# Kernel optimization log

Measured on AMD Instinct MI355X. Metric: run time of the kernel, lower is better.

Reference implementation:

```python
import jax, jax.numpy as jnp
import numpy as np

N, H, K, B, L = 8192, 256, 128, 64, 128


def setup_inputs() -> dict:
    key = jax.random.key(0)
    ks = jax.random.split(key, 12)
    s_emb = 1.0 / np.sqrt(H)
    return {
        "A": jax.random.normal(ks[0], (N, N), jnp.float32) * 0.02,           # dense adjacency
        "emb": jax.random.normal(ks[1], (N, H), jnp.float32) * s_emb,        # GCN embedding
        "Wc": jax.random.normal(ks[2], (H, H), jnp.float32) * s_emb,         # Conv1d k=1 (multi_gram)
        "bc": jnp.zeros((H,), jnp.float32),
        "W1": jax.random.normal(ks[3], (K, 2 * H), jnp.float32) * 0.05,      # Conv2d fs=1, width=2H
        "b1": jnp.zeros((K,), jnp.float32),
        "W2": jax.random.normal(ks[4], (K, 2, 2 * H), jnp.float32) * 0.05,   # Conv2d fs=2
        "b2": jnp.zeros((K,), jnp.float32),
        "Wd": jax.random.normal(ks[5], (2, 4 * K), jnp.float32) * 0.05,      # dense
        "bd": jnp.zeros((2,), jnp.float32),
        "q_idx": jax.random.randint(ks[6], (B, L), 0, N, jnp.int32),
        "a_idx": jax.random.randint(ks[7], (B, L), 0, N, jnp.int32),
    }


def reference(A, emb, Wc, bc, W1, b1, W2, b2, Wd, bd, q_idx, a_idx):
    # GCN layer (featureless): layer1 = A @ embedding  -> [N, H]
    layer1 = A @ emb

    # padded per-sample word gather + multi_gram (kernel-1 conv == rowwise linear + ReLU)
    def gram(idx):
        x = jnp.take(layer1, idx, axis=0)                      # [B, L, H]
        return jax.nn.relu(jnp.einsum("blh,oh->blo", x, Wc) + bc)

    Qm = gram(q_idx)                                           # [B, L, H]
    Am = gram(a_idx)                                           # [B, L, H]

    # soft cross attention
    s = jnp.einsum("bqh,bkh->bqk", Qm, Am)                     # [B, Lq, La]
    eq = jnp.einsum("bqk,bkh->bqh", jax.nn.softmax(s, axis=-1), Am)
    ea = jnp.einsum("bkq,bqh->bkh", jax.nn.softmax(jnp.swapaxes(s, 1, 2), axis=-1), Qm)

    # full-width conv2d encoders over [L, 2H] feature map, max-pooled over L
    def encode(X, E):
        t = jnp.concatenate([(X - E) ** 2, X * E], axis=-1)    # [B, L, 2H]
        e1 = jax.nn.relu(jnp.einsum("bld,kd->blk", t, W1) + b1).max(axis=1)      # fs=1 -> [B, K]
        e2 = jax.nn.relu(
            jnp.einsum("bld,kd->blk", t[:, :-1], W2[:, 0])
            + jnp.einsum("bld,kd->blk", t[:, 1:], W2[:, 1])
            + b2
        ).max(axis=1)                                          # fs=2 -> [B, K]
        return jax.nn.relu(jnp.concatenate([e1, e2], axis=-1)) # [B, 2K] (dropout = identity in eval)

    re = jnp.concatenate([encode(Qm, eq), encode(Am, ea)], axis=-1)  # [B, 4K]
    return jax.nn.log_softmax(re @ Wd.T + bd, axis=-1)          # [B, 2]
```

## Files before the change

kernel.cpp:

```cpp
#include <hip/hip_runtime.h>
#include <hip/hip_bf16.h>
#include <math.h>

#define NN 8192
#define HH 256
#define BB 64
#define LL 128
#define SPLITK 4

typedef __attribute__((ext_vector_type(8))) short short8v;
typedef __attribute__((ext_vector_type(4))) short short4v;
typedef __attribute__((ext_vector_type(4))) float f32x4;

static __device__ inline short bf16bits(float f) {
    __hip_bfloat16 h = __float2bfloat16(f);
    return __builtin_bit_cast(short, h);
}
static __device__ inline float bits2f(short s) {
    __hip_bfloat16 h = __builtin_bit_cast(__hip_bfloat16, s);
    return __bfloat162float(h);
}
static __device__ inline short8v cvt8(float4 f0, float4 f1) {
    short8v r;
    r[0] = bf16bits(f0.x); r[1] = bf16bits(f0.y);
    r[2] = bf16bits(f0.z); r[3] = bf16bits(f0.w);
    r[4] = bf16bits(f1.x); r[5] = bf16bits(f1.y);
    r[6] = bf16bits(f1.z); r[7] = bf16bits(f1.w);
    return r;
}
static __device__ inline void glds16(const void* src, void* lds) {
    __builtin_amdgcn_global_load_lds(
        (const __attribute__((address_space(1))) void*)src,
        (__attribute__((address_space(3))) void*)lds, 16, 0, 0);
}
template<int N> static __device__ inline void vmwait() {
    if constexpr (N == 0)  asm volatile("s_waitcnt vmcnt(0)"  ::: "memory");
    else if constexpr (N == 1)  asm volatile("s_waitcnt vmcnt(1)"  ::: "memory");
    else if constexpr (N == 2)  asm volatile("s_waitcnt vmcnt(2)"  ::: "memory");
    else if constexpr (N == 3)  asm volatile("s_waitcnt vmcnt(3)"  ::: "memory");
    else if constexpr (N == 4)  asm volatile("s_waitcnt vmcnt(4)"  ::: "memory");
    else if constexpr (N == 5)  asm volatile("s_waitcnt vmcnt(5)"  ::: "memory");
    else if constexpr (N == 6)  asm volatile("s_waitcnt vmcnt(6)"  ::: "memory");
    else if constexpr (N == 7)  asm volatile("s_waitcnt vmcnt(7)"  ::: "memory");
    else if constexpr (N == 8)  asm volatile("s_waitcnt vmcnt(8)"  ::: "memory");
    else                        asm volatile("s_waitcnt vmcnt(12)" ::: "memory");
}
static __device__ inline void lgkm0_barrier() {
    asm volatile("s_waitcnt lgkmcnt(0)" ::: "memory");
    __builtin_amdgcn_s_barrier();
    __builtin_amdgcn_sched_barrier(0);
}


__global__ __launch_bounds__(256) void prep(
    const float* __restrict__ emb, short* __restrict__ embT,
    const float* __restrict__ Wc, short* __restrict__ Wcb,
    const float* __restrict__ W1, const float* __restrict__ W2,
    short* __restrict__ WcatT)
{
    __shared__ short tile[64][65];
    const int bid = blockIdx.x;
    const int t = threadIdx.x;
    if (bid < 512) {
        const int k0 = (bid & 127) * 64, h0 = (bid >> 7) * 64;
#pragma unroll
        for (int i = 0; i < 16; i++) {
            int idx = t + i * 256;
            int k = idx >> 6, h = idx & 63;
            tile[h][k] = bf16bits(emb[(long)(k0 + k) * 256 + h0 + h]);
        }
        __syncthreads();
#pragma unroll
        for (int i = 0; i < 16; i++) {
            int idx = t + i * 256;
            int h = idx >> 6, k = idx & 63;
            int n = h0 + h;
            int kk = (k0 + k) ^ ((n & 3) << 3);
            embT[(long)n * NN + kk] = tile[h][k];
        }
    } else {
        int i = (bid - 512) * 256 + t;
        if (i < 256 * 256) {
            int n = i >> 8, c = i & 255;
            Wcb[n * 256 + (c ^ ((n & 3) << 3))] = bf16bits(Wc[i]);
        }
        if (i < 384 * 512) {
            int n = i >> 9, d = i & 511;
            float v;
            if (n < 128)      v = W1[n * 512 + d];
            else if (n < 256) v = W2[(n - 128) * 1024 + d];
            else              v = W2[(n - 256) * 1024 + 512 + d];
            WcatT[n * 512 + (d ^ ((n & 3) << 3))] = bf16bits(v);
        }
    }
}

__global__ __launch_bounds__(512, 4) void l1_gemm(
    const float* __restrict__ Af, const short* __restrict__ Bt,
    short* __restrict__ Part)
{
    constexpr int AST = 40;

    __shared__ short As[2][128 * AST];
    __shared__ short Bs[3][256 * 32];

    const int tid = threadIdx.x;
    const int wave = tid >> 6, lane = tid & 63;
    const int wr = wave >> 2, wc = wave & 3;
    const int r16 = lane & 15, kg = lane >> 4;

    const int sk = blockIdx.x & 3, mt = blockIdx.x >> 2;
    const int m0 = mt * 128;
    const int kbeg = sk * 2048;
    constexpr int NIT = 64;

    const int arow = tid >> 2;
    const int akc = (tid & 3) * 8;
    const long arow_g = (long)(m0 + arow) * NN;

    f32x4 acc[4][4] = {};

#define STAGE_B(T, BUF)                                                        \
    {                                                                          \
        const int kt_ = kbeg + (T) * 32;                                       \
        _Pragma("unroll")                                                      \
        for (int c = 0; c < 2; c++) {                                          \
            int chunk = c * 512 + tid;                                         \
            int n_ = chunk >> 2, kc_ = (chunk & 3) * 8;                        \
            glds16(Bt + (long)n_ * NN + kt_ + kc_,                             \
                   &Bs[BUF][(c * 512 + wave * 64) * 8]);                       \
        }                                                                      \
    }
#define LOAD_A(T, F0, F1)                                                      \
    {                                                                          \
        const float* ap_ = Af + arow_g + kbeg + (T) * 32 + akc;                \
        (F0) = *(const float4*)ap_; (F1) = *(const float4*)(ap_ + 4);          \
    }
#define WRITE_A(BUF, F0, F1) { *(short8v*)&As[BUF][arow * AST + akc] = cvt8((F0), (F1)); }

    float4 p0f0, p0f1, c1f0, c1f1;
    LOAD_A(0, p0f0, p0f1);  STAGE_B(0, 0);
    LOAD_A(1, c1f0, c1f1);  STAGE_B(1, 1);
    WRITE_A(0, p0f0, p0f1);
    vmwait<4>();
    lgkm0_barrier();

    for (int t = 0; t < NIT; ++t) {
        const int curA = t & 1, nwA = (t + 1) & 1;
        const int curB = t % 3, nsB = (t + 2) % 3;
        float4 nf0, nf1;
        if (t + 2 < NIT) {
            LOAD_A(t + 2, nf0, nf1);
            STAGE_B(t + 2, nsB);
        }

        short8v a[4], b[4];
#pragma unroll
        for (int i = 0; i < 4; i++)
            a[i] = *(const short8v*)&As[curA][(wr * 64 + i * 16 + r16) * AST + kg * 8];
#pragma unroll
        for (int j = 0; j < 4; j++) {
            int n = wc * 64 + j * 16 + r16;
            b[j] = *(const short8v*)&Bs[curB][n * 32 + ((kg * 8) ^ ((n & 3) << 3))];
        }
#pragma unroll
        for (int i = 0; i < 4; i++)
#pragma unroll
            for (int j = 0; j < 4; j++)
                acc[i][j] = __builtin_amdgcn_mfma_f32_16x16x32_bf16(
                    a[i], b[j], acc[i][j], 0, 0, 0);

        if (t + 1 < NIT) {
            WRITE_A(nwA, c1f0, c1f1);
            if (t + 2 < NIT) vmwait<4>();
            else             vmwait<0>();
            lgkm0_barrier();
        }
        c1f0 = nf0; c1f1 = nf1;
    }
#undef STAGE_B
#undef LOAD_A
#undef WRITE_A

    short* P = Part + (long)sk * NN * HH;
#pragma unroll
    for (int i = 0; i < 4; i++)
#pragma unroll
        for (int j = 0; j < 4; j++) {
            int col = wc * 64 + j * 16 + r16;
#pragma unroll
            for (int r = 0; r < 4; r++) {
                int row = m0 + wr * 64 + i * 16 + kg * 4 + r;
                P[(long)row * HH + col] = bf16bits(acc[i][j][r]);
            }
        }
}

__global__ __launch_bounds__(256) void reduceK(
    const short* __restrict__ P, short* __restrict__ out)
{
    const long n = (long)NN * HH;
    long i = ((long)blockIdx.x * 256 + threadIdx.x) * 8;
    if (i >= n) return;
    float acc[8] = {};
#pragma unroll
    for (int k = 0; k < SPLITK; k++) {
        short8v v = *(const short8v*)&P[(long)k * n + i];
#pragma unroll
        for (int j = 0; j < 8; j++) acc[j] += bits2f(v[j]);
    }
    short8v o;
#pragma unroll
    for (int j = 0; j < 8; j++) o[j] = bf16bits(acc[j]);
    *(short8v*)&out[i] = o;
}

template<int NW, int NT, int GATHER, int EPI>
__global__ __launch_bounds__(256) void gemm_small(
    const short* __restrict__ Aq, const short* __restrict__ Aa,
    const short* __restrict__ Bt,
    float* __restrict__ Cfq, float* __restrict__ Cfa,
    short* __restrict__ Cbq, short* __restrict__ Cba,
    short* __restrict__ Ctq, short* __restrict__ Cta,
    const float* __restrict__ bias,
    const int* __restrict__ idxq, const int* __restrict__ idxa,
    int M, int N, int Kd)
{
    constexpr int BM = 64;
    constexpr int BN = NW * 4;
    constexpr int NB = NW / 16;
    constexpr int BCALLS = BN / BM;
    constexpr int OPS = 1 + BCALLS;
    constexpr int AST = 40;

    __shared__ short As[4][BM * AST];
    __shared__ short Bs[4][BN * 32];

    const int tid = threadIdx.x;
    const int wave = tid >> 6, lane = tid & 63;
    const int wc = wave & 3;
    const int r16 = lane & 15, kg = lane >> 4;

    const int bid = blockIdx.x;
    const int side = bid & 1;
    const int nt = (bid >> 1) & (NT - 1);
    const int mt = bid >> (NT == 2 ? 2 : 1);
    const int m0 = mt * BM;
    const int n0 = nt * BN;
    const int niter = Kd / 32;

    const short* Ab = side ? Aa : Aq;
    const int* rowidx = side ? idxa : idxq;

    const int arow = tid >> 2;
    const int akc = (tid & 3) * 8;
    long arow_g;
    { int r = GATHER ? rowidx[m0 + arow] : (m0 + arow); arow_g = (long)r * Kd; }

    f32x4 acc[4][NB] = {};

#define STAGE_B(T, BUF)                                                        \
    {                                                                          \
        const int kt_ = (T) * 32;                                              \
        _Pragma("unroll")                                                      \
        for (int c = 0; c < BCALLS; c++) {                                     \
            int chunk = c * 256 + tid;                                         \
            int n_ = chunk >> 2, kc_ = (chunk & 3) * 8;                        \
            glds16(Bt + (long)(n0 + n_) * Kd + kt_ + kc_,                      \
                   &Bs[BUF][(c * 256 + wave * 64) * 8]);                       \
        }                                                                      \
    }
#define LOAD_A(T, AR)  { (AR) = *(const short8v*)(Ab + arow_g + (T) * 32 + akc); }
#define WRITE_A(BUF, AR) { *(short8v*)&As[BUF][arow * AST + akc] = (AR); }

    short8v a0, a1, a2;
    LOAD_A(0, a0);  STAGE_B(0, 0);
    LOAD_A(1, a1);  STAGE_B(1, 1);
    LOAD_A(2, a2);  STAGE_B(2, 2);
    WRITE_A(0, a0);
    vmwait<2 * OPS>();
    lgkm0_barrier();

    for (int t = 0; t < niter; ++t) {
        const int cur = t & 3, nw = (t + 1) & 3, ns = (t + 3) & 3;
        short8v na;
        if (t + 3 < niter) {
            LOAD_A(t + 3, na);
            STAGE_B(t + 3, ns);
        }

        short8v a[4], b[NB];
#pragma unroll
        for (int i = 0; i < 4; i++)
            a[i] = *(const short8v*)&As[cur][(i * 16 + r16) * AST + kg * 8];
#pragma unroll
        for (int j = 0; j < NB; j++) {
            int n = wc * NW + j * 16 + r16;
            b[j] = *(const short8v*)&Bs[cur][n * 32 + ((kg * 8) ^ ((n & 3) << 3))];
        }
#pragma unroll
        for (int i = 0; i < 4; i++)
#pragma unroll
            for (int j = 0; j < NB; j++)
                acc[i][j] = __builtin_amdgcn_mfma_f32_16x16x32_bf16(
                    a[i], b[j], acc[i][j], 0, 0, 0);

        if (t + 1 < niter) {
            WRITE_A(nw, a1);
            if (t + 3 < niter)      vmwait<2 * OPS>();
            else if (t + 2 < niter) vmwait<OPS>();
            else                    vmwait<0>();
            lgkm0_barrier();
        }
        a1 = a2; a2 = na;
    }
#undef STAGE_B
#undef LOAD_A
#undef WRITE_A

    if (EPI == 2) {
        float* Cf = side ? Cfa : Cfq;
#pragma unroll
        for (int i = 0; i < 4; i++)
#pragma unroll
            for (int j = 0; j < NB; j++) {
                int col = n0 + wc * NW + j * 16 + r16;
#pragma unroll
                for (int r = 0; r < 4; r++) {
                    int row = m0 + i * 16 + kg * 4 + r;
                    Cf[(long)row * N + col] = acc[i][j][r];
                }
            }
    } else {
        short* Cb = side ? Cba : Cbq;
        short* Ct = side ? Cta : Ctq;
#pragma unroll
        for (int i = 0; i < 4; i++)
#pragma unroll
            for (int j = 0; j < NB; j++) {
                int col = n0 + wc * NW + j * 16 + r16;
                float bv = bias[col];
                float vr[4];
#pragma unroll
                for (int r = 0; r < 4; r++)
                    vr[r] = fmaxf(acc[i][j][r] + bv, 0.f);
                int rbase = m0 + i * 16 + kg * 4;
                int bb = rbase >> 7;
                int lbase = rbase & 127;
#pragma unroll
                for (int r = 0; r < 4; r++) {
                    int grow = rbase + r;
                    Cb[(long)grow * 256 + (col ^ ((grow & 7) << 3))] = bf16bits(vr[r]);
                }
                short4v t4;
#pragma unroll
                for (int r = 0; r < 4; r++) t4[r] = bf16bits(vr[r]);
                int lsw = lbase ^ ((col & 7) << 3);
                *(short4v*)&Ct[(long)bb * (256 * 128) + col * 128 + lsw] = t4;
            }
    }
}

__global__ __launch_bounds__(256) void qkT(
    const short* __restrict__ Qb16, const short* __restrict__ Ab16,
    float* __restrict__ s)
{
    __shared__ short Q[64 * 256];
    __shared__ short Am[128 * 256];
    const int b = blockIdx.x >> 1;
    const int qh = blockIdx.x & 1;
    const int tid = threadIdx.x, wave = tid >> 6, lane = tid & 63;
    const int r16 = lane & 15, kg = lane >> 4;
    const long boff = (long)b * 128 * 256;
    const long qoff = boff + (long)qh * 64 * 256;

#pragma unroll
    for (int c = 0; c < 8; c++)
        glds16(Qb16 + qoff + ((long)c * 256 + tid) * 8, &Q[(c * 256 + wave * 64) * 8]);
#pragma unroll
    for (int c = 0; c < 16; c++)
        glds16(Ab16 + boff + ((long)c * 256 + tid) * 8, &Am[(c * 256 + wave * 64) * 8]);
    __syncthreads();

    f32x4 acc[8] = {};
    const int q0 = wave * 16;
#pragma unroll
    for (int ks = 0; ks < 8; ks++) {
        short8v a;
        {
            int q = q0 + r16;
            a = *(const short8v*)&Q[q * 256 + ((ks * 32 + kg * 8) ^ ((q & 7) << 3))];
        }
#pragma unroll
        for (int j = 0; j < 8; j++) {
            int n = j * 16 + r16;
            short8v bf = *(const short8v*)&Am[n * 256 + ((ks * 32 + kg * 8) ^ ((n & 7) << 3))];
            acc[j] = __builtin_amdgcn_mfma_f32_16x16x32_bf16(a, bf, acc[j], 0, 0, 0);
        }
    }

    float* sp = s + (long)b * 16384 + (long)qh * 64 * 128;
#pragma unroll
    for (int j = 0; j < 8; j++)
#pragma unroll
        for (int r = 0; r < 4; r++) {
            int q = q0 + kg * 4 + r;
            int k = j * 16 + r16;
            sp[q * 128 + k] = acc[j][r];
        }
}

__global__ __launch_bounds__(256) void attn_pv(
    const float* __restrict__ s,
    const short* __restrict__ AT, const short* __restrict__ QT,
    const short* __restrict__ Qb16, const short* __restrict__ Ab16,
    short* __restrict__ t_q, short* __restrict__ t_a)
{
    __shared__ short XL[256 * 128];
    __shared__ float sm[64 * 128];
    __shared__ short P[64 * 128];
    const int b = blockIdx.x >> 2;
    const int side = (blockIdx.x >> 1) & 1;
    const int h = blockIdx.x & 1;
    const int tid = threadIdx.x, wave = tid >> 6, lane = tid & 63;
    const int r16 = lane & 15, kg = lane >> 4;

    const short* XT   = side ? QT : AT;
    const short* Xrow = side ? Ab16 : Qb16;
    short* tout       = side ? t_a : t_q;

#pragma unroll
    for (int c = 0; c < 16; c++)
        glds16(XT + (long)b * 32768 + ((long)c * 256 + tid) * 8,
               &XL[(c * 256 + wave * 64) * 8]);
    if (side == 0) {
#pragma unroll
        for (int c = 0; c < 8; c++)
            glds16(s + (long)b * 16384 + (long)h * 8192 + ((long)c * 256 + tid) * 4,
                   &sm[(c * 256 + wave * 64) * 4]);
    } else {
#pragma unroll
        for (int c = 0; c < 8; c++) {
            int idx = c * 256 + tid;
            int q = idx >> 4, off = (idx & 15) * 4;
            glds16(s + (long)b * 16384 + (long)q * 128 + h * 64 + off,
                   &sm[(c * 256 + wave * 64) * 4]);
        }
    }
    __syncthreads();

    {
        const int r = tid >> 2;
        const int qt = tid & 3;
        float mx = -1e30f;
#pragma unroll 8
        for (int i = 0; i < 32; i++) {
            int k = qt * 32 + ((i + r) & 31);
            float v = (side == 0) ? sm[r * 128 + k] : sm[k * 64 + r];
            mx = fmaxf(mx, v);
        }
        mx = fmaxf(mx, __shfl_xor(mx, 1));
        mx = fmaxf(mx, __shfl_xor(mx, 2));
        float sum = 0.f;
#pragma unroll 8
        for (int i = 0; i < 32; i++) {
            int k = qt * 32 + ((i + r) & 31);
            float v = (side == 0) ? sm[r * 128 + k] : sm[k * 64 + r];
            sum += __expf(v - mx);
        }
        sum += __shfl_xor(sum, 1);
        sum += __shfl_xor(sum, 2);
        float inv = 1.f / sum;
#pragma unroll 8
        for (int i = 0; i < 32; i++) {
            int k = qt * 32 + ((i + r) & 31);
            float v = (side == 0) ? sm[r * 128 + k] : sm[k * 64 + r];
            P[r * 128 + (k ^ ((r & 7) << 3))] = bf16bits(__expf(v - mx) * inv);
        }
    }
    __syncthreads();

    f32x4 acc[4][4] = {};
#pragma unroll
    for (int ks = 0; ks < 4; ks++) {
        short8v a[4], bf[4];
#pragma unroll
        for (int i = 0; i < 4; i++) {
            int row = i * 16 + r16;
            a[i] = *(const short8v*)&P[row * 128 + ((ks * 32 + kg * 8) ^ ((row & 7) << 3))];
        }
#pragma unroll
        for (int j = 0; j < 4; j++) {
            int hh = wave * 64 + j * 16 + r16;
            bf[j] = *(const short8v*)&XL[hh * 128 + ((ks * 32 + kg * 8) ^ ((hh & 7) << 3))];
        }
#pragma unroll
        for (int i = 0; i < 4; i++)
#pragma unroll
            for (int j = 0; j < 4; j++)
                acc[i][j] = __builtin_amdgcn_mfma_f32_16x16x32_bf16(
                    a[i], bf[j], acc[i][j], 0, 0, 0);
    }

    short* tp = tout + (long)b * 128 * 512 + (long)h * 64 * 512;
    const short* xr = Xrow + (long)b * 128 * 256 + (long)h * 64 * 256;
#pragma unroll
    for (int i = 0; i < 4; i++)
#pragma unroll
        for (int j = 0; j < 4; j++) {
            int col = wave * 64 + j * 16 + r16;
#pragma unroll
            for (int r = 0; r < 4; r++) {
                int row = i * 16 + kg * 4 + r;
                float E = acc[i][j][r];
                float x = bits2f(xr[row * 256 + (col ^ ((row & 7) << 3))]);
                float d = x - E;
                tp[(long)row * 512 + col] = bf16bits(d * d);
                tp[(long)row * 512 + 256 + col] = bf16bits(x * E);
            }
        }
}

__global__ __launch_bounds__(512) void pool_final(
    const float* __restrict__ u_q, const float* __restrict__ u_a,
    const float* __restrict__ b1, const float* __restrict__ b2,
    const float* __restrict__ Wd, const float* __restrict__ bd,
    float* __restrict__ out)
{
    __shared__ float re[512];
    const int b = blockIdx.x;
    const int t = threadIdx.x;
    const int side = t >> 8;
    const int kk = t & 255;
    const float* uu = side ? u_a : u_q;
    if (kk < 128) {
        int k = kk;
        float bias = b1[k];
        float mx = -1e30f;
        for (int l = 0; l < 128; l++) {
            float v = uu[((long)b * 128 + l) * 384 + k] + bias;
            mx = fmaxf(mx, v);
        }
        re[side * 256 + k] = fmaxf(mx, 0.f);
    } else {
        int k = kk - 128;
        float bias = b2[k];
        float mx = -1e30f;
        for (int l = 0; l < 127; l++) {
            float v = uu[((long)b * 128 + l) * 384 + 128 + k]
                    + uu[((long)b * 128 + l + 1) * 384 + 256 + k] + bias;
            mx = fmaxf(mx, v);
        }
        re[side * 256 + 128 + k] = fmaxf(mx, 0.f);
    }
    __syncthreads();
    if (t < 64) {
        float p0 = 0.f, p1 = 0.f;
        for (int d = t; d < 512; d += 64) {
            float r = re[d];
            p0 = fmaf(r, Wd[d], p0);
            p1 = fmaf(r, Wd[512 + d], p1);
        }
#pragma unroll
        for (int off = 32; off; off >>= 1) {
            p0 += __shfl_xor(p0, off);
            p1 += __shfl_xor(p1, off);
        }
        if (t == 0) {
            float l0 = p0 + bd[0], l1 = p1 + bd[1];
            float m = fmaxf(l0, l1);
            float lse = m + logf(expf(l0 - m) + expf(l1 - m));
            out[b * 2 + 0] = l0 - lse;
            out[b * 2 + 1] = l1 - lse;
        }
    }
}

extern "C" void kernel_launch(void* const* d_in, const int* in_sizes, int n_in,
                              void* d_out, int out_size, void* d_ws, size_t ws_size,
                              hipStream_t stream)
{
    const float* A    = (const float*)d_in[0];
    const float* emb  = (const float*)d_in[1];
    const float* Wc   = (const float*)d_in[2];
    const float* bc   = (const float*)d_in[3];
    const float* W1   = (const float*)d_in[4];
    const float* b1   = (const float*)d_in[5];
    const float* W2   = (const float*)d_in[6];
    const float* b2   = (const float*)d_in[7];
    const float* Wd   = (const float*)d_in[8];
    const float* bd   = (const float*)d_in[9];
    const int* q_idx  = (const int*)d_in[10];
    const int* a_idx  = (const int*)d_in[11];
    float* out = (float*)d_out;
    float* ws  = (float*)d_ws;

    const long SZ_L1 = (long)NN * HH;
    float* p      = ws;
    short* Part   = (short*)p;          p += (long)SPLITK * SZ_L1 / 2;
    short* l1b    = (short*)p;          p += SZ_L1 / 2 + 1024;
    short* Wcb    = (short*)p;          p += 32768 + 1024;
    short* WcatT  = (short*)p;          p += 98304 + 1024;
    short* embT   = (short*)p;          p += SZ_L1 / 2 + 1024;
    short* Qb16   = (short*)p;          p += SZ_L1 / 2 + 1024;
    short* Ab16   = (short*)p;          p += SZ_L1 / 2 + 1024;
    short* QT     = (short*)p;          p += SZ_L1 / 2 + 1024;
    short* AT     = (short*)p;          p += SZ_L1 / 2 + 1024;
    float* s      = p;                  p += (long)BB * LL * LL;
    short* t_q    = (short*)p;          p += SZ_L1 + 1024;
    short* t_a    = (short*)p;          p += SZ_L1 + 1024;
    float* u_q    = p;                  p += (long)BB * LL * 384;
    float* u_a    = p;                  p += (long)BB * LL * 384;

    prep<<<1280, 256, 0, stream>>>(emb, embT, Wc, Wcb, W1, W2, WcatT);

    l1_gemm<<<256, 512, 0, stream>>>(A, embT, Part);
    reduceK<<<(int)(SZ_L1 / 8 / 256), 256, 0, stream>>>(Part, l1b);

    gemm_small<32, 2, 1, 1><<<512, 256, 0, stream>>>(
        l1b, l1b, Wcb, nullptr, nullptr, Qb16, Ab16, QT, AT, bc,
        q_idx, a_idx, BB * LL, HH, HH);

    qkT<<<2 * BB, 256, 0, stream>>>(Qb16, Ab16, s);
    attn_pv<<<4 * BB, 256, 0, stream>>>(s, AT, QT, Qb16, Ab16, t_q, t_a);

    gemm_small<48, 2, 0, 2><<<512, 256, 0, stream>>>(
        t_q, t_a, WcatT, u_q, u_a, nullptr, nullptr, nullptr, nullptr, nullptr,
        nullptr, nullptr, BB * LL, 384, 512);

    pool_final<<<BB, 512, 0, stream>>>(u_q, u_a, b1, b2, Wd, bd, out);
}
```

Measured before the change: 176.3 us.

## Stage fp32 A tiles via direct global-to-LDS loads with 4-stage pipeline

The A operand (fp32 adjacency) is no longer loaded into registers, converted to bf16 and written to LDS. It is now copied straight into LDS with async global-to-LDS loads in an XOR-swizzled layout and converted to bf16 when the fragments are read. The pipeline grows from 2/3 buffers to 4 stages with a 3-deep prefetch, and launch bounds drop to 2 blocks per CU. The aim is to remove register staging and the VGPR pressure of holding A in flight. The cost is doubled LDS for A, repeated conversion by every wave that reads the tile, and lower occupancy.

After: 198.5 us. 1.13x slower.

```diff
diff --git a/kernel.cpp b/kernel.cpp
--- a/kernel.cpp
+++ b/kernel.cpp
@@ -95,14 +95,12 @@
     }
 }
 
-__global__ __launch_bounds__(512, 4) void l1_gemm(
+__global__ __launch_bounds__(512, 2) void l1_gemm(
     const float* __restrict__ Af, const short* __restrict__ Bt,
     short* __restrict__ Part)
 {
-    constexpr int AST = 40;
-
-    __shared__ short As[2][128 * AST];
-    __shared__ short Bs[3][256 * 32];
+    __shared__ float Asf[4][128 * 32];
+    __shared__ short Bs[4][256 * 32];
 
     const int tid = threadIdx.x;
     const int wave = tid >> 6, lane = tid & 63;
@@ -114,54 +112,47 @@
     const int kbeg = sk * 2048;
     constexpr int NIT = 64;
 
-    const int arow = tid >> 2;
-    const int akc = (tid & 3) * 8;
-    const long arow_g = (long)(m0 + arow) * NN;
-
     f32x4 acc[4][4] = {};
 
-#define STAGE_B(T, BUF)                                                        \
+#define STAGE(T, BUF)                                                          \
     {                                                                          \
         const int kt_ = kbeg + (T) * 32;                                       \
         _Pragma("unroll")                                                      \
         for (int c = 0; c < 2; c++) {                                          \
             int chunk = c * 512 + tid;                                         \
+            int arow_ = chunk >> 3, apos_ = chunk & 7;                         \
+            int aj_ = apos_ ^ (arow_ & 7);                                     \
+            glds16(Af + (long)(m0 + arow_) * NN + kt_ + aj_ * 4,               \
+                   &Asf[BUF][(c * 512 + wave * 64) * 4]);                      \
             int n_ = chunk >> 2, kc_ = (chunk & 3) * 8;                        \
             glds16(Bt + (long)n_ * NN + kt_ + kc_,                             \
                    &Bs[BUF][(c * 512 + wave * 64) * 8]);                       \
         }                                                                      \
     }
-#define LOAD_A(T, F0, F1)                                                      \
-    {                                                                          \
-        const float* ap_ = Af + arow_g + kbeg + (T) * 32 + akc;                \
-        (F0) = *(const float4*)ap_; (F1) = *(const float4*)(ap_ + 4);          \
-    }
-#define WRITE_A(BUF, F0, F1) { *(short8v*)&As[BUF][arow * AST + akc] = cvt8((F0), (F1)); }
-
-    float4 p0f0, p0f1, c1f0, c1f1;
-    LOAD_A(0, p0f0, p0f1);  STAGE_B(0, 0);
-    LOAD_A(1, c1f0, c1f1);  STAGE_B(1, 1);
-    WRITE_A(0, p0f0, p0f1);
-    vmwait<4>();
+
+    STAGE(0, 0);
+    STAGE(1, 1);
+    STAGE(2, 2);
+    vmwait<8>();
     lgkm0_barrier();
 
     for (int t = 0; t < NIT; ++t) {
-        const int curA = t & 1, nwA = (t + 1) & 1;
-        const int curB = t % 3, nsB = (t + 2) % 3;
-        float4 nf0, nf1;
-        if (t + 2 < NIT) {
-            LOAD_A(t + 2, nf0, nf1);
-            STAGE_B(t + 2, nsB);
-        }
+        const int cur = t & 3;
+        if (t + 3 < NIT) STAGE(t + 3, (t + 3) & 3);
 
         short8v a[4], b[4];
 #pragma unroll
-        for (int i = 0; i < 4; i++)
-            a[i] = *(const short8v*)&As[curA][(wr * 64 + i * 16 + r16) * AST + kg * 8];
+        for (int i = 0; i < 4; i++) {
+            int row = wr * 64 + i * 16 + r16;
+            int p0 = (2 * kg) ^ (row & 7), p1 = (2 * kg + 1) ^ (row & 7);
+            float4 f0 = *(const float4*)&Asf[cur][row * 32 + p0 * 4];
+            float4 f1 = *(const float4*)&Asf[cur][row * 32 + p1 * 4];
+            a[i] = cvt8(f0, f1);
+        }
 #pragma unroll
         for (int j = 0; j < 4; j++) {
             int n = wc * 64 + j * 16 + r16;
-            b[j] = *(const short8v*)&Bs[curB][n * 32 + ((kg * 8) ^ ((n & 3) << 3))];
+            b[j] = *(const short8v*)&Bs[cur][n * 32 + ((kg * 8) ^ ((n & 3) << 3))];
         }
 #pragma unroll
         for (int i = 0; i < 4; i++)
@@ -171,16 +162,13 @@
                     a[i], b[j], acc[i][j], 0, 0, 0);
 
         if (t + 1 < NIT) {
-            WRITE_A(nwA, c1f0, c1f1);
-            if (t + 2 < NIT) vmwait<4>();
-            else             vmwait<0>();
+            if (t + 3 < NIT)      vmwait<8>();
+            else if (t + 2 < NIT) vmwait<4>();
+            else                  vmwait<0>();
             lgkm0_barrier();
         }
-        c1f0 = nf0; c1f1 = nf1;
-    }
-#undef STAGE_B
-#undef LOAD_A
-#undef WRITE_A
+    }
+#undef STAGE
 
     short* P = Part + (long)sk * NN * HH;
 #pragma unroll
```
